# Performance work log

Measured on AMD Instinct MI355X. Metric: run time of the kernel, lower is better.

## Reference

```python
import jax, jax.numpy as jnp
import numpy as np

NB_STEPS = 50
ALPHA = 0.9
NUM_RNN_STEPS = 2
B = 4096
NUM_FEATURE = 100
IN_D = 5
HIDDEN = [64, 64, 64]
P1 = (1.1, 1.1, 1.5, 2.0, 2.5)   # IntegrandNN_outer_level powers
P2 = (1.5, 2.0, 2.5, 3.0, 3.5)   # IntegrandNN powers


def _cc(nb_steps):
    # Clenshaw-Curtis weights/steps, identical to UMNN's compute_cc_weights
    n = nb_steps
    i = np.arange(n + 1, dtype=np.float64).reshape(-1, 1)
    lam = np.cos(i @ i.T * np.pi / n)
    lam[:, 0] = 0.5
    lam[:, -1] *= 0.5
    lam = lam * 2.0 / n
    W = np.zeros(n + 1)
    even = np.arange(0, n + 1, 2)
    W[even] = 2.0 / (1.0 - even.astype(np.float64) ** 2)
    W[0] = 1.0
    ccw = (lam.T @ W).astype(np.float32)                         # [n+1]
    steps = np.cos(np.arange(n + 1) * np.pi / n).astype(np.float32)  # [n+1]
    return jnp.asarray(ccw), jnp.asarray(steps)

CC_W, CC_S = _cc(NB_STEPS)


def _mlp(xh, Ws, bs):
    # Linear+ReLU stack with ELU on the last layer (ReLU popped, ELU appended)
    h = xh
    for W, b in zip(Ws[:-1], bs[:-1]):
        h = jax.nn.relu(h @ W.T + b)
    return jax.nn.elu(h @ Ws[-1].T + bs[-1])


def _integrand(x, h, Ws, bs, Wf, powers):
    z = _mlp(jnp.concatenate([x, h], axis=1), Ws, bs) + 1.0      # [N,1], z >= 0
    feats = jnp.concatenate([z ** p for p in powers], axis=1)    # [N,5]
    return jax.nn.relu((1.0 / (feats + 1.0)) @ Wf.T)             # [N,1]


def _integrate(x0, xT, h, f):
    # ParallelNeuralIntegral forward: CC quadrature of f from x0 to xT
    Bn, S = x0.shape[0], NB_STEPS + 1
    X = x0[:, None, :] + (xT - x0)[:, None, :] * (CC_S[None, :, None] + 1.0) / 2.0  # [B,S,1]
    hs = jnp.broadcast_to(h[:, None, :], (Bn, S, h.shape[1])).reshape(-1, h.shape[1])
    dz = f(X.reshape(-1, 1), hs).reshape(Bn, S, 1)
    return (dz * CC_W[None, :, None]).sum(1) * (xT - x0) / 2.0   # [B,1]


def setup_inputs() -> dict:
    key = jax.random.key(0)
    ks = jax.random.split(key, 24)
    def lin(k, o, i):
        return jax.random.normal(k, (o, i), jnp.float32) / np.sqrt(i)
    d = {}
    d["x_"] = jax.random.normal(ks[0], (B, NUM_FEATURE), jnp.float32)
    d["h_"] = jax.random.normal(ks[1], (B, IN_D - 1), jnp.float32)
    d["log_weight"] = jnp.ones((1, NUM_FEATURE), jnp.float32)     # reset_parameters -> 1
    d["sigmoid_param"] = jnp.zeros((1,), jnp.float32)
    sizes = [IN_D] + HIDDEN + [1]
    for tag, base in (("f1", 2), ("f2", 12)):
        for li, (i, o) in enumerate(zip(sizes[:-1], sizes[1:])):
            d[f"{tag}_W{li}"] = lin(ks[base + 2 * li], o, i)
            d[f"{tag}_b{li}"] = jnp.zeros((o,), jnp.float32)
        d[f"{tag}_Wf"] = jnp.abs(lin(ks[base + 9], 1, 5))         # reset_params -> abs
    return d


def reference(x_, h_, log_weight, sigmoid_param,
              f1_W0, f1_b0, f1_W1, f1_b1, f1_W2, f1_b2, f1_W3, f1_b3, f1_Wf,
              f2_W0, f2_b0, f2_W1, f2_b1, f2_W2, f2_b2, f2_W3, f2_b3, f2_Wf):
    f1Ws = [f1_W0, f1_W1, f1_W2, f1_W3]; f1bs = [f1_b0, f1_b1, f1_b2, f1_b3]
    f2Ws = [f2_W0, f2_W1, f2_W2, f2_W3]; f2bs = [f2_b0, f2_b1, f2_b2, f2_b3]
    f1 = lambda x, h: _integrand(x, h, f1Ws, f1bs, f1_Wf, P1)
    f2 = lambda x, h: _integrand(x, h, f2Ws, f2bs, f2_Wf, P2)

    # modular function: linear to [B,1] then sum over dim 1 -> [B,1]
    xm = jnp.sum(x_ * log_weight[0], axis=1, keepdims=True)
    lam = jax.nn.sigmoid(sigmoid_param[0])

    I1 = jnp.zeros_like(xm)
    I2 = jnp.zeros_like(xm)
    out_first = None
    for _ in range(NUM_RNN_STEPS):
        x = (1.0 - lam) * xm + lam * I1
        x2 = (1.0 - lam) * xm + lam * I2
        out_first = f1(x2, h_)
        I1 = _integrate(jnp.zeros_like(x), x, h_, f1)
        xmax = jnp.max(x2) + 10.0
        xfinal = jnp.zeros_like(x) + xmax
        I2 = (1.0 / ALPHA) * _integrate(x2, xfinal, h_, f2)
    return I1, out_first, I2
```

## Files before the change

kernel.cpp:

```cpp
#include <hip/hip_runtime.h>
#include <math.h>

typedef _Float16 half8v __attribute__((ext_vector_type(8)));
typedef _Float16 half4v __attribute__((ext_vector_type(4)));
typedef _Float16 half2v __attribute__((ext_vector_type(2)));
typedef float float4v __attribute__((ext_vector_type(4)));

#define BB    4096
#define INV_ALPHA (1.0f/0.9f)

#define WS_CCW  0
#define WS_CCS  64
#define WS_LAM  128
#define WS_PM16 160
#define WS_PM   256
#define WS_XM   512
#define WS_X    (WS_XM + BB)
#define WS_X2   (WS_X + BB)
#define WS_H    16384
#define H_NET   8192
#define H_W2    4096
#define H_W0    16384
#define H_W3    20480

#if defined(__has_builtin)
#if __has_builtin(__builtin_amdgcn_rcpf)
#define FRCP(x) __builtin_amdgcn_rcpf(x)
#endif
#if __has_builtin(__builtin_amdgcn_exp2f)
#define FEXP2(x) __builtin_amdgcn_exp2f(x)
#endif
#if __has_builtin(__builtin_amdgcn_logf)
#define FLOG2(x) __builtin_amdgcn_logf(x)
#endif
#endif
#ifndef FRCP
#define FRCP(x) (1.0f / (x))
#endif
#ifndef FEXP2
#define FEXP2(x) exp2f(x)
#endif
#ifndef FLOG2
#define FLOG2(x) log2f(x)
#endif

__device__ __forceinline__ int swz(int row, int cb) {
    return (row << 6) + (((cb ^ (row & 7)) & 7) << 3);
}

__device__ __forceinline__ half4v pk_relu4(float4v c) {
#if defined(__has_builtin) && __has_builtin(__builtin_amdgcn_cvt_pkrtz)
    half2v a = __builtin_bit_cast(half2v,
        __builtin_amdgcn_cvt_pkrtz(fmaxf(c[0], 0.0f), fmaxf(c[1], 0.0f)));
    half2v b = __builtin_bit_cast(half2v,
        __builtin_amdgcn_cvt_pkrtz(fmaxf(c[2], 0.0f), fmaxf(c[3], 0.0f)));
    half4v o; o[0] = a[0]; o[1] = a[1]; o[2] = b[0]; o[3] = b[1];
    return o;
#else
    half4v o;
    o[0] = (_Float16)fmaxf(c[0], 0.0f); o[1] = (_Float16)fmaxf(c[1], 0.0f);
    o[2] = (_Float16)fmaxf(c[2], 0.0f); o[3] = (_Float16)fmaxf(c[3], 0.0f);
    return o;
#endif
}

__device__ __forceinline__ float tail5(float y,
        float p0, float p1, float p2, float p3, float p4,
        float wf0, float wf1, float wf2, float wf3, float wf4) {
    if (y <= 0.0f) y = FEXP2(y * 1.44269504f) - 1.0f;
    float z = y + 1.0f;
    float lg = FLOG2(z);
    float g = wf0 * FRCP(FEXP2(p0 * lg) + 1.0f)
            + wf1 * FRCP(FEXP2(p1 * lg) + 1.0f)
            + wf2 * FRCP(FEXP2(p2 * lg) + 1.0f)
            + wf3 * FRCP(FEXP2(p3 * lg) + 1.0f)
            + wf4 * FRCP(FEXP2(p4 * lg) + 1.0f);
    return fmaxf(g, 0.0f);
}

__global__ void k_setup(const float* __restrict__ x_, const float* __restrict__ lw,
                        const float* __restrict__ sp,
                        const float* __restrict__ f1W0, const float* __restrict__ f1W1,
                        const float* __restrict__ f1W2, const float* __restrict__ f1W3,
                        const float* __restrict__ f2W0, const float* __restrict__ f2W1,
                        const float* __restrict__ f2W2, const float* __restrict__ f2W3,
                        float* __restrict__ ws, float* __restrict__ out) {
    _Float16* wh = (_Float16*)(ws + WS_H);
    const int blk = blockIdx.x, tid = threadIdx.x;
    if (blk < 256) {
        int wave = tid >> 6, lane = tid & 63;
        float vmax = -1e30f;
        for (int r = 0; r < 4; ++r) {
            int row = blk * 16 + wave * 4 + r;
            float v = 0.0f;
            for (int i = lane; i < 100; i += 64) v = fmaf(x_[row * 100 + i], lw[i], v);
            #pragma unroll
            for (int off = 32; off > 0; off >>= 1) v += __shfl_xor(v, off, 64);
            if (lane == 0) ws[WS_XM + row] = v;
            vmax = fmaxf(vmax, v);
        }
        __shared__ float sm[4];
        if (lane == 0) sm[wave] = vmax;
        __syncthreads();
        if (tid == 0)
            ws[WS_PM + blk] = fmaxf(fmaxf(sm[0], sm[1]), fmaxf(sm[2], sm[3]));
    } else if (blk < 272) {
        int t = (blk - 256) * 256 + tid;
        wh[t]                = (_Float16)f1W1[t];
        wh[H_W2 + t]         = (_Float16)f1W2[t];
        wh[H_NET + t]        = (_Float16)f2W1[t];
        wh[H_NET + H_W2 + t] = (_Float16)f2W2[t];
        if (t < 2048) {
            int j = t >> 5, k = t & 31;
            wh[H_W0 + t]        = (k < 5) ? (_Float16)f1W0[j * 5 + k] : (_Float16)0.0f;
            wh[H_W0 + 2048 + t] = (k < 5) ? (_Float16)f2W0[j * 5 + k] : (_Float16)0.0f;
        }
        if (t < 64) {
            wh[H_W3 + t]      = (_Float16)f1W3[t];
            wh[H_W3 + 64 + t] = (_Float16)f2W3[t];
        }
    } else if (blk == 272) {
        if (tid == 64) ws[WS_LAM] = 1.0f / (1.0f + expf(-sp[0]));
        if (tid <= 50) {
            int s = tid;
            ws[WS_CCS + s] = cospif((float)s / 50.0f);
            float acc = 0.0f;
            for (int a = 0; a <= 50; ++a) {
                float w;
                if (a == 0) w = 1.0f;
                else if ((a & 1) == 0) w = 2.0f / (1.0f - (float)(a * a));
                else continue;
                float l;
                if (s == 0) l = 0.5f;
                else {
                    int m = (a * s) % 100;
                    l = cospif((float)m / 50.0f);
                    if (s == 50) l *= 0.5f;
                }
                acc += l * 0.04f * w;
            }
            ws[WS_CCW + s] = acc;
        }
    } else {
        int t = (blk - 273) * 256 + tid;
        out[t < BB ? t : BB + t] = 0.0f;
    }
}

__global__ void k_pre(float* __restrict__ ws, float* __restrict__ out) {
    int b = blockIdx.x * 256 + threadIdx.x;
    float lam = ws[WS_LAM];
    float m = ws[WS_XM + b];
    float xv  = (1.0f - lam) * m + lam * out[b];
    float x2v = (1.0f - lam) * m + lam * out[2 * BB + b];
    ws[WS_X + b] = xv;
    ws[WS_X2 + b] = x2v;
    out[b] = 0.0f;
    out[2 * BB + b] = 0.0f;
    __shared__ float red[256];
    red[threadIdx.x] = x2v;
    __syncthreads();
    #pragma unroll
    for (int off = 128; off > 0; off >>= 1) {
        if (threadIdx.x < off)
            red[threadIdx.x] = fmaxf(red[threadIdx.x], red[threadIdx.x + off]);
        __syncthreads();
    }
    if (threadIdx.x == 0) ws[WS_PM16 + blockIdx.x] = red[0];
}

__global__ __launch_bounds__(256, 2) void k_int(
    int mode, float* __restrict__ ws, const float* __restrict__ h_,
    const float* __restrict__ f1b0, const float* __restrict__ f1b1,
    const float* __restrict__ f1b2, const float* __restrict__ f1b3,
    const float* __restrict__ f1Wf,
    const float* __restrict__ f2b0, const float* __restrict__ f2b1,
    const float* __restrict__ f2b2, const float* __restrict__ f2b3,
    const float* __restrict__ f2Wf,
    float* __restrict__ out)
{
    __shared__ _Float16 act[4 * 64 * 64];
    __shared__ _Float16 w0f[4 * 16 * 8];
    __shared__ _Float16 w1f[512 * 8];
    __shared__ _Float16 w2f[512 * 8];
    __shared__ float bl[192];

    const int tid = threadIdx.x;
    const int blk = blockIdx.x;
    const int wloc = tid >> 6;
    const int lane = tid & 63;
    const int lo = lane & 15, q = lane >> 4;

    const int g = blk >> 3;
    const int w = (blk & 7) * 4 + wloc;
    const bool u2 = (g >= 64);
    const int base = (g & 63) << 6;
    const bool of_wave = (mode != 0) && (!u2) && (w == 31);

    const float* xm = ws + WS_XM;
    const float* xarr = ws + WS_X;
    const float* x2arr = ws + WS_X2;
    const _Float16* wh = (const _Float16*)(ws + WS_H);
    const float lam = ws[WS_LAM];
    const float oml = 1.0f - lam;

    const _Float16* W0h = wh + H_W0 + (u2 ? 2048 : 0);
    const _Float16* W1h = wh + (u2 ? H_NET : 0);
    const _Float16* W2h = W1h + H_W2;
    const _Float16* W3h = wh + H_W3 + (u2 ? 64 : 0);
    const float* B0 = u2 ? f2b0 : f1b0;
    const float* B1 = u2 ? f2b1 : f1b1;
    const float* B2 = u2 ? f2b2 : f1b2;
    const float* B3 = u2 ? f2b3 : f1b3;
    const float* WF = u2 ? f2Wf : f1Wf;
    const float p0 = u2 ? 1.5f : 1.1f;
    const float p1 = u2 ? 2.0f : 1.1f;
    const float p2 = u2 ? 2.5f : 1.5f;
    const float p3 = u2 ? 3.0f : 2.0f;
    const float p4 = u2 ? 3.5f : 2.5f;

    #pragma unroll
    for (int f = tid; f < 512; f += 256) {
        int fm = f >> 7, fkb = (f >> 6) & 1, fl = f & 63;
        int flo = fl & 15, fq = fl >> 4;
        *(half8v*)(w1f + f * 8) =
            *(const half8v*)(W1h + (16 * fm + flo) * 64 + fkb * 32 + fq * 8);
        *(half8v*)(w2f + f * 8) =
            *(const half8v*)(W2h + (16 * fm + flo) * 64 + fkb * 32 + fq * 8);
    }
    if (tid < 64) {
        int fm = tid >> 4, flo = tid & 15;
        *(half8v*)(w0f + tid * 8) = *(const half8v*)(W0h + (16 * fm + flo) * 32);
    }
    if (tid < 192)
        bl[tid] = (tid < 64) ? B0[tid] : (tid < 128) ? B1[tid - 64] : B2[tid - 128];

    half4v w3r[4];
    #pragma unroll
    for (int m = 0; m < 4; ++m)
        w3r[m] = *(const half4v*)(W3h + 16 * m + 4 * q);
    const float B3s = B3[0];
    const float wf0 = WF[0], wf1 = WF[1], wf2 = WF[2], wf3 = WF[3], wf4 = WF[4];

    half8v zf;
    #pragma unroll
    for (int t2 = 0; t2 < 8; ++t2) zf[t2] = (_Float16)0.0f;

    float xr_r[4], x2_r[4];
    half8v tpl[4];
    #pragma unroll
    for (int n = 0; n < 4; ++n) {
        int idx = base + 16 * n + lo;
        xr_r[n] = mode ? (u2 ? x2arr[idx] : xarr[idx]) : oml * xm[idx];
        float4 h4 = ((const float4*)h_)[idx];
        half8v e = zf;
        e[1] = (_Float16)h4.x; e[2] = (_Float16)h4.y;
        e[3] = (_Float16)h4.z; e[4] = (_Float16)h4.w;
        tpl[n] = (q == 0) ? e : zf;
        x2_r[n] = 0.0f;
    }
    if (of_wave) {
        #pragma unroll
        for (int n = 0; n < 4; ++n) x2_r[n] = x2arr[base + 16 * n + lo];
    }

    float xmax = 0.0f;
    if (u2) {
        if (mode) {
            float v = (lane < 16) ? ws[WS_PM16 + lane] : -1e30f;
            #pragma unroll
            for (int off = 32; off > 0; off >>= 1) v = fmaxf(v, __shfl_xor(v, off, 64));
            xmax = v + 10.0f;
        } else {
            const float* pm = ws + WS_PM;
            float v = fmaxf(fmaxf(pm[lane], pm[lane + 64]),
                            fmaxf(pm[lane + 128], pm[lane + 192]));
            #pragma unroll
            for (int off = 32; off > 0; off >>= 1) v = fmaxf(v, __shfl_xor(v, off, 64));
            xmax = oml * v + 10.0f;
        }
    }

    __syncthreads();

    _Float16* actw = act + (wloc << 12);
    const int np = (w <= 18 || of_wave) ? 2 : 1;
    float acc = 0.0f;

    #pragma clang loop unroll(disable)
    for (int p = 0; p < np; ++p) {
        const bool of_iter = of_wave && (p == 1);
        float t = 0.0f, ccw_s = 0.0f;
        if (!of_iter) {
            int s = w + 32 * p;
            t = (ws[WS_CCS + s] + 1.0f) * 0.5f;
            ccw_s = ws[WS_CCW + s];
        }

        half8v Bf0[4];
        #pragma unroll
        for (int n = 0; n < 4; ++n) {
            float xin;
            if (of_iter) xin = x2_r[n];
            else if (u2) xin = fmaf(t, xmax - xr_r[n], xr_r[n]);
            else         xin = xr_r[n] * t;
            half8v b = tpl[n];
            b[0] = (_Float16)((q == 0) ? xin : 0.0f);
            Bf0[n] = b;
        }

        #pragma unroll
        for (int m = 0; m < 4; ++m) {
            half8v a0 = (q == 0) ? *(const half8v*)(w0f + (m * 16 + lo) * 8) : zf;
            float4v b0 = *(const float4v*)(bl + 16 * m + 4 * q);
            #pragma unroll
            for (int n = 0; n < 4; ++n) {
                float4v c = __builtin_amdgcn_mfma_f32_16x16x32_f16(a0, Bf0[n], b0, 0, 0, 0);
                *(half4v*)(actw + swz(16 * n + lo, 2 * m + (q >> 1)) + 4 * (q & 1)) = pk_relu4(c);
            }
        }

        {
            half8v Bf[2][4];
            #pragma unroll
            for (int kb = 0; kb < 2; ++kb)
                #pragma unroll
                for (int n = 0; n < 4; ++n)
                    Bf[kb][n] = *(const half8v*)(actw + swz(16 * n + lo, 4 * kb + q));
            #pragma unroll
            for (int m = 0; m < 4; ++m) {
                half8v a10 = *(const half8v*)(w1f + ((m * 2 + 0) * 64 + lane) * 8);
                half8v a11 = *(const half8v*)(w1f + ((m * 2 + 1) * 64 + lane) * 8);
                float4v b1 = *(const float4v*)(bl + 64 + 16 * m + 4 * q);
                #pragma unroll
                for (int n = 0; n < 4; ++n) {
                    float4v c = __builtin_amdgcn_mfma_f32_16x16x32_f16(a10, Bf[0][n], b1, 0, 0, 0);
                    c = __builtin_amdgcn_mfma_f32_16x16x32_f16(a11, Bf[1][n], c, 0, 0, 0);
                    *(half4v*)(actw + swz(16 * n + lo, 2 * m + (q >> 1)) + 4 * (q & 1)) = pk_relu4(c);
                }
            }
        }

        float part[4] = {0.0f, 0.0f, 0.0f, 0.0f};
        {
            half8v Bf[2][4];
            #pragma unroll
            for (int kb = 0; kb < 2; ++kb)
                #pragma unroll
                for (int n = 0; n < 4; ++n)
                    Bf[kb][n] = *(const half8v*)(actw + swz(16 * n + lo, 4 * kb + q));
            #pragma unroll
            for (int m = 0; m < 4; ++m) {
                half8v a20 = *(const half8v*)(w2f + ((m * 2 + 0) * 64 + lane) * 8);
                half8v a21 = *(const half8v*)(w2f + ((m * 2 + 1) * 64 + lane) * 8);
                float4v b2 = *(const float4v*)(bl + 128 + 16 * m + 4 * q);
                #pragma unroll
                for (int n = 0; n < 4; ++n) {
                    float4v c = __builtin_amdgcn_mfma_f32_16x16x32_f16(a20, Bf[0][n], b2, 0, 0, 0);
                    c = __builtin_amdgcn_mfma_f32_16x16x32_f16(a21, Bf[1][n], c, 0, 0, 0);
                    #pragma unroll
                    for (int e = 0; e < 4; ++e)
                        part[n] = fmaf((float)w3r[m][e], fmaxf(c[e], 0.0f), part[n]);
                }
            }
        }

        #pragma unroll
        for (int n = 0; n < 4; ++n) {
            part[n] += __shfl_xor(part[n], 16, 64);
            part[n] += __shfl_xor(part[n], 32, 64);
        }
        float y = B3s + (q == 0 ? part[0] : q == 1 ? part[1] : q == 2 ? part[2] : part[3]);

        float val = tail5(y, p0, p1, p2, p3, p4, wf0, wf1, wf2, wf3, wf4);

        if (of_iter) out[BB + base + lane] = val;
        else         acc = fmaf(ccw_s, val, acc);
    }

    const float x_l = (q == 0 ? xr_r[0] : q == 1 ? xr_r[1] : q == 2 ? xr_r[2] : xr_r[3]);
    if (!u2) {
        atomicAdd(out + base + lane, acc * x_l * 0.5f);
    } else {
        atomicAdd(out + 2 * BB + base + lane, acc * (xmax - x_l) * 0.5f * INV_ALPHA);
    }
}

extern "C" void kernel_launch(void* const* d_in, const int* in_sizes, int n_in,
                              void* d_out, int out_size, void* d_ws, size_t ws_size,
                              hipStream_t stream) {
    const float* x_  = (const float*)d_in[0];
    const float* h_  = (const float*)d_in[1];
    const float* lw  = (const float*)d_in[2];
    const float* sp  = (const float*)d_in[3];
    const float* f1W0 = (const float*)d_in[4];   const float* f1b0 = (const float*)d_in[5];
    const float* f1W1 = (const float*)d_in[6];   const float* f1b1 = (const float*)d_in[7];
    const float* f1W2 = (const float*)d_in[8];   const float* f1b2 = (const float*)d_in[9];
    const float* f1W3 = (const float*)d_in[10];  const float* f1b3 = (const float*)d_in[11];
    const float* f1Wf = (const float*)d_in[12];
    const float* f2W0 = (const float*)d_in[13];  const float* f2b0 = (const float*)d_in[14];
    const float* f2W1 = (const float*)d_in[15];  const float* f2b1 = (const float*)d_in[16];
    const float* f2W2 = (const float*)d_in[17];  const float* f2b2 = (const float*)d_in[18];
    const float* f2W3 = (const float*)d_in[19];  const float* f2b3 = (const float*)d_in[20];
    const float* f2Wf = (const float*)d_in[21];
    float* out = (float*)d_out;
    float* ws  = (float*)d_ws;

    k_setup<<<305, 256, 0, stream>>>(x_, lw, sp,
                                     f1W0, f1W1, f1W2, f1W3,
                                     f2W0, f2W1, f2W2, f2W3, ws, out);
    k_int<<<1024, 256, 0, stream>>>(0, ws, h_,
        f1b0, f1b1, f1b2, f1b3, f1Wf, f2b0, f2b1, f2b2, f2b3, f2Wf, out);
    k_pre<<<16, 256, 0, stream>>>(ws, out);
    k_int<<<1024, 256, 0, stream>>>(1, ws, h_,
        f1b0, f1b1, f1b2, f1b3, f1Wf, f2b0, f2b1, f2b2, f2b3, f2Wf, out);
}
```

Before: 142.2 us.

## Fold inter-step prep into last-block epilogue and repartition quadrature steps per wave

Removes the separate k_pre launch. The first integration pass accumulates into workspace buffers, and the last block to finish, found with an atomic counter, computes x, x2 and the global max of x2 for the second pass. The grid also shrinks from 1024 to 768 blocks, with each wave handling 2–3 quadrature steps instead of 1–2, and launch bounds rise to 3 blocks per SM. This trades one kernel launch and a more balanced step split for a serial tail in which a single block processes all 4096 elements, plus higher register pressure.

```diff
diff --git a/kernel.cpp b/kernel.cpp
--- a/kernel.cpp
+++ b/kernel.cpp
@@ -12,12 +12,15 @@
 #define WS_CCW  0
 #define WS_CCS  64
 #define WS_LAM  128
-#define WS_PM16 160
+#define WS_CNT  132
+#define WS_XMX2 133
 #define WS_PM   256
 #define WS_XM   512
 #define WS_X    (WS_XM + BB)
 #define WS_X2   (WS_X + BB)
-#define WS_H    16384
+#define WS_A1   (WS_X2 + BB)
+#define WS_A2   (WS_A1 + BB)
+#define WS_H    24576
 #define H_NET   8192
 #define H_W2    4096
 #define H_W0    16384
@@ -121,6 +124,7 @@
         }
     } else if (blk == 272) {
         if (tid == 64) ws[WS_LAM] = 1.0f / (1.0f + expf(-sp[0]));
+        if (tid == 63) ws[WS_CNT] = 0.0f;
         if (tid <= 50) {
             int s = tid;
             ws[WS_CCS + s] = cospif((float)s / 50.0f);
@@ -141,35 +145,16 @@
             }
             ws[WS_CCW + s] = acc;
         }
-    } else {
+    } else if (blk < 305) {
         int t = (blk - 273) * 256 + tid;
         out[t < BB ? t : BB + t] = 0.0f;
-    }
-}
-
-__global__ void k_pre(float* __restrict__ ws, float* __restrict__ out) {
-    int b = blockIdx.x * 256 + threadIdx.x;
-    float lam = ws[WS_LAM];
-    float m = ws[WS_XM + b];
-    float xv  = (1.0f - lam) * m + lam * out[b];
-    float x2v = (1.0f - lam) * m + lam * out[2 * BB + b];
-    ws[WS_X + b] = xv;
-    ws[WS_X2 + b] = x2v;
-    out[b] = 0.0f;
-    out[2 * BB + b] = 0.0f;
-    __shared__ float red[256];
-    red[threadIdx.x] = x2v;
-    __syncthreads();
-    #pragma unroll
-    for (int off = 128; off > 0; off >>= 1) {
-        if (threadIdx.x < off)
-            red[threadIdx.x] = fmaxf(red[threadIdx.x], red[threadIdx.x + off]);
-        __syncthreads();
-    }
-    if (threadIdx.x == 0) ws[WS_PM16 + blockIdx.x] = red[0];
-}
-
-__global__ __launch_bounds__(256, 2) void k_int(
+    } else {
+        int t = (blk - 305) * 256 + tid;
+        ws[WS_A1 + t] = 0.0f;
+    }
+}
+
+__global__ __launch_bounds__(256, 3) void k_int(
     int mode, float* __restrict__ ws, const float* __restrict__ h_,
     const float* __restrict__ f1b0, const float* __restrict__ f1b1,
     const float* __restrict__ f1b2, const float* __restrict__ f1b3,
@@ -191,11 +176,11 @@
     const int lane = tid & 63;
     const int lo = lane & 15, q = lane >> 4;
 
-    const int g = blk >> 3;
-    const int w = (blk & 7) * 4 + wloc;
+    const int g = blk / 6;
+    const int w = (blk - g * 6) * 4 + wloc;
     const bool u2 = (g >= 64);
     const int base = (g & 63) << 6;
-    const bool of_wave = (mode != 0) && (!u2) && (w == 31);
+    const bool of_wave = (mode != 0) && (!u2) && (w == 23);
 
     const float* xm = ws + WS_XM;
     const float* xarr = ws + WS_X;
@@ -267,10 +252,7 @@
     float xmax = 0.0f;
     if (u2) {
         if (mode) {
-            float v = (lane < 16) ? ws[WS_PM16 + lane] : -1e30f;
-            #pragma unroll
-            for (int off = 32; off > 0; off >>= 1) v = fmaxf(v, __shfl_xor(v, off, 64));
-            xmax = v + 10.0f;
+            xmax = ws[WS_XMX2] + 10.0f;
         } else {
             const float* pm = ws + WS_PM;
             float v = fmaxf(fmaxf(pm[lane], pm[lane + 64]),
@@ -284,15 +266,15 @@
     __syncthreads();
 
     _Float16* actw = act + (wloc << 12);
-    const int np = (w <= 18 || of_wave) ? 2 : 1;
+    const int np = (w < 3 || of_wave) ? 3 : 2;
     float acc = 0.0f;
 
     #pragma clang loop unroll(disable)
     for (int p = 0; p < np; ++p) {
-        const bool of_iter = of_wave && (p == 1);
+        const bool of_iter = of_wave && (p == 2);
         float t = 0.0f, ccw_s = 0.0f;
         if (!of_iter) {
-            int s = w + 32 * p;
+            int s = w + 24 * p;
             t = (ws[WS_CCS + s] + 1.0f) * 0.5f;
             ccw_s = ws[WS_CCW + s];
         }
@@ -379,10 +361,46 @@
     }
 
     const float x_l = (q == 0 ? xr_r[0] : q == 1 ? xr_r[1] : q == 2 ? xr_r[2] : xr_r[3]);
-    if (!u2) {
-        atomicAdd(out + base + lane, acc * x_l * 0.5f);
+    if (mode == 0) {
+        if (!u2) atomicAdd(ws + WS_A1 + base + lane, acc * x_l * 0.5f);
+        else     atomicAdd(ws + WS_A2 + base + lane, acc * (xmax - x_l) * 0.5f * INV_ALPHA);
+
+        __threadfence();
+        __syncthreads();
+        __shared__ bool last;
+        if (tid == 0) {
+            unsigned* cnt = (unsigned*)(ws + WS_CNT);
+            last = (atomicAdd(cnt, 1u) == (unsigned)(gridDim.x - 1));
+        }
+        __syncthreads();
+        if (last) {
+            __threadfence();
+            float vmax = -1e30f;
+            for (int i = tid; i < BB; i += 256) {
+                float a1 = __hip_atomic_load(ws + WS_A1 + i, __ATOMIC_RELAXED,
+                                             __HIP_MEMORY_SCOPE_AGENT);
+                float a2 = __hip_atomic_load(ws + WS_A2 + i, __ATOMIC_RELAXED,
+                                             __HIP_MEMORY_SCOPE_AGENT);
+                float m0 = xm[i];
+                float xv  = oml * m0 + lam * a1;
+                float x2v = oml * m0 + lam * a2;
+                ws[WS_X + i]  = xv;
+                ws[WS_X2 + i] = x2v;
+                vmax = fmaxf(vmax, x2v);
+            }
+            #pragma unroll
+            for (int off = 32; off > 0; off >>= 1)
+                vmax = fmaxf(vmax, __shfl_xor(vmax, off, 64));
+            __shared__ float rm[4];
+            if (lane == 0) rm[wloc] = vmax;
+            __syncthreads();
+            if (tid == 0)
+                ws[WS_XMX2] = fmaxf(fmaxf(rm[0], rm[1]), fmaxf(rm[2], rm[3]));
+        }
     } else {
-        atomicAdd(out + 2 * BB + base + lane, acc * (xmax - x_l) * 0.5f * INV_ALPHA);
+        if (!u2) atomicAdd(out + base + lane, acc * x_l * 0.5f);
+        else     atomicAdd(out + 2 * BB + base + lane,
+                           acc * (xmax - x_l) * 0.5f * INV_ALPHA);
     }
 }
 
@@ -406,12 +424,11 @@
     float* out = (float*)d_out;
     float* ws  = (float*)d_ws;
 
-    k_setup<<<305, 256, 0, stream>>>(x_, lw, sp,
+    k_setup<<<337, 256, 0, stream>>>(x_, lw, sp,
                                      f1W0, f1W1, f1W2, f1W3,
                                      f2W0, f2W1, f2W2, f2W3, ws, out);
-    k_int<<<1024, 256, 0, stream>>>(0, ws, h_,
+    k_int<<<768, 256, 0, stream>>>(0, ws, h_,
         f1b0, f1b1, f1b2, f1b3, f1Wf, f2b0, f2b1, f2b2, f2b3, f2Wf, out);
-    k_pre<<<16, 256, 0, stream>>>(ws, out);
-    k_int<<<1024, 256, 0, stream>>>(1, ws, h_,
+    k_int<<<768, 256, 0, stream>>>(1, ws, h_,
         f1b0, f1b1, f1b2, f1b3, f1Wf, f2b0, f2b1, f2b2, f2b3, f2Wf, out);
 }
```

Measured after the change: 279.4 us. 96.4% more time.
